# Kernel optimization log

Hardware: AMD Instinct MI355X
Metric: run time of the kernel (lower is better)

## Reference

```python
import jax, jax.numpy as jnp
import numpy as np

N = 50000      # nodes
E = 800000     # edges (before self-loops)
G = 64         # graphs
F_IN = 128     # n_attr
OUT = 128      # size_vect
NEG_SLOPE = 0.2


def setup_inputs() -> dict:
    key = jax.random.key(0)
    ks = jax.random.split(key, 48)
    def rn(i, shape, s=0.05):
        return (jax.random.normal(ks[i], shape, jnp.float32) * s)
    x = jax.random.normal(ks[0], (N, F_IN), jnp.float32)
    src = jax.random.randint(ks[1], (E,), 0, N, jnp.int32)
    dst = jax.random.randint(ks[2], (E,), 0, N, jnp.int32)
    dst = jnp.where(dst == src, (dst + 1) % N, dst)  # no pre-existing self-loops
    edge_index = jnp.stack([src, dst])
    batch = jnp.sort(jax.random.randint(ks[3], (N,), 0, G, jnp.int32))
    inp = {"x": x, "edge_index": edge_index, "batch": batch}
    # GATConv params (heads=1): W [in,out], att_src/att_dst [out], bias [out]
    dims = [(F_IN, 64), (64, 128), (128, 256)]
    for li, (di, do) in enumerate(dims, start=1):
        b = 4 + (li - 1) * 4
        inp[f"W{li}"] = rn(b, (di, do))
        inp[f"asrc{li}"] = rn(b + 1, (do,))
        inp[f"adst{li}"] = rn(b + 2, (do,))
        inp[f"b{li}"] = rn(b + 3, (do,))
    # dense tail: Linear stored as [in,out]
    dense = {"d1": (512, 256), "d2": (256, 128), "d3": (128, 64),
             "mean": (256, 64), "d4": (64, 64), "d5": (64, 128),
             "d6": (128, 256), "d7": (256, OUT)}
    i = 20
    for name, (di, do) in dense.items():
        inp[f"{name}_w"] = rn(i, (di, do))
        inp[f"{name}_b"] = rn(i + 1, (do,))
        i += 2
    return inp


def _gat_conv(x, src, dst, W, a_src, a_dst, b):
    h = x @ W                                   # [N, out]
    e = (h @ a_src)[src] + (h @ a_dst)[dst]     # [E']
    e = jnp.where(e > 0, e, NEG_SLOPE * e)      # LeakyReLU(0.2)
    m = jax.ops.segment_max(e, dst, num_segments=N)
    ex = jnp.exp(e - m[dst])
    denom = jax.ops.segment_sum(ex, dst, num_segments=N)
    alpha = ex / denom[dst]                     # segment softmax over incoming edges
    out = jax.ops.segment_sum(h[src] * alpha[:, None], dst, num_segments=N)
    return out + b


def reference(x, edge_index, batch,
              W1, asrc1, adst1, b1, W2, asrc2, adst2, b2, W3, asrc3, adst3, b3,
              d1_w, d1_b, d2_w, d2_b, d3_w, d3_b, mean_w, mean_b,
              d4_w, d4_b, d5_w, d5_b, d6_w, d6_b, d7_w, d7_b):
    ar = jnp.arange(N, dtype=edge_index.dtype)
    src = jnp.concatenate([edge_index[0], ar])  # add self-loops (PyG default)
    dst = jnp.concatenate([edge_index[1], ar])
    h = _gat_conv(x, src, dst, W1, asrc1, adst1, b1)
    h = _gat_conv(h, src, dst, W2, asrc2, adst2, b2)
    h = _gat_conv(h, src, dst, W3, asrc3, adst3, b3)   # [N, 256]
    x1 = jax.ops.segment_max(h, batch, num_segments=G)
    x2 = jax.ops.segment_sum(h, batch, num_segments=G)
    cnt = jax.ops.segment_sum(jnp.ones((N,), h.dtype), batch, num_segments=G)
    x3 = x2 / jnp.maximum(cnt, 1.0)[:, None]
    z = jnp.concatenate([x1, x2], axis=-1)              # [G, 512]
    z = jax.nn.relu(z @ d1_w + d1_b)
    z = jax.nn.relu(z @ d2_w + d2_b)
    z = jax.nn.relu(z @ d3_w + d3_b)
    z = z * jax.nn.sigmoid(x3 @ mean_w + mean_b)
    z = jax.nn.relu(z @ d4_w + d4_b)                    # dropout = identity (eval)
    z = jax.nn.relu(z @ d5_w + d5_b)
    z = jax.nn.relu(z @ d6_w + d6_b)
    return z @ d7_w + d7_b
```

## Files before the change

kernel.cpp:

```cpp
#include <hip/hip_runtime.h>
#include <hip/hip_bf16.h>
#include <math.h>

#define NN 50000
#define NE 800000
#define NEP 850000
#define NG 64
#define CAP 64

#define NBKT 49
#define BMAX 20480
#define EPB  3125
#define KE   13

typedef unsigned short u16;
typedef __attribute__((ext_vector_type(8))) short short8;
typedef __attribute__((ext_vector_type(4))) float f32x4;

__device__ __forceinline__ float bfu2f(u16 u) {
    return __uint_as_float((unsigned)u << 16);
}
__device__ __forceinline__ u16 f2bfu(float f) {
    __hip_bfloat16 h = __float2bfloat16(f);
    union { __hip_bfloat16 h; u16 u; } c; c.h = h; return c.u;
}

__device__ __forceinline__ unsigned fkey(float f) {
    unsigned u = __float_as_uint(f);
    return (u & 0x80000000u) ? ~u : (u | 0x80000000u);
}
__device__ __forceinline__ float fkey_inv(unsigned k) {
    return (k & 0x80000000u) ? __uint_as_float(k ^ 0x80000000u) : __uint_as_float(~k);
}

__global__ void k_init(int* __restrict__ deg, u16* __restrict__ srcsort,
                       int* __restrict__ poolbuf, int IB,
                       const float* __restrict__ W0, const float* __restrict__ as0, const float* __restrict__ ad0,
                       u16* __restrict__ Wb0, float* __restrict__ wa0, float* __restrict__ wb0,
                       const float* __restrict__ W1, const float* __restrict__ as1, const float* __restrict__ ad1,
                       u16* __restrict__ Wb1, float* __restrict__ wa1, float* __restrict__ wb1,
                       const float* __restrict__ W2, const float* __restrict__ as2, const float* __restrict__ ad2,
                       const float* __restrict__ b2f, const float* __restrict__ b3f,
                       u16* __restrict__ Wcb, float* __restrict__ bcv,
                       float* __restrict__ wa2c, float* __restrict__ wb2c,
                       float* __restrict__ cst) {
    __shared__ float pas[4], pbs[4];
    int tid = threadIdx.x;
    if (blockIdx.x < IB) {
        int i = blockIdx.x * 256 + tid;
        if (i < NN) {
            deg[i] = 1;
            srcsort[i << 6] = (u16)i;
        } else if (i - NN < NG * 512 + NG + 64) {
            poolbuf[i - NN] = 0;
        }
        return;
    }
    int b = blockIdx.x - IB;
    if (b < 192) {
        const float *W, *asv, *adv; u16* Wb; float *wa, *wb; int k, dout;
        if (b < 128) { W = W0; asv = as0; adv = ad0; Wb = Wb0; wa = wa0; wb = wb0; k = b;       dout = 64;  }
        else         { W = W1; asv = as1; adv = ad1; Wb = Wb1; wa = wa1; wb = wb1; k = b - 128; dout = 128; }
        float pa = 0.f, pb = 0.f;
        for (int n = tid; n < dout; n += 256) {
            float w = W[(size_t)k * dout + n];
            Wb[(size_t)k * dout + n] = f2bfu(w);
            pa += w * asv[n];
            pb += w * adv[n];
        }
#pragma unroll
        for (int off = 32; off; off >>= 1) {
            pa += __shfl_xor(pa, off);
            pb += __shfl_xor(pb, off);
        }
        if ((tid & 63) == 0) { pas[tid >> 6] = pa; pbs[tid >> 6] = pb; }
        __syncthreads();
        if (tid == 0) {
            wa[k] = pas[0] + pas[1] + pas[2] + pas[3];
            wb[k] = pbs[0] + pbs[1] + pbs[2] + pbs[3];
        }
        return;
    }
    if (b < 256) {
        int k = b - 192;
        int o = tid;
        float wc = 0.f;
        const float* wrow = W1 + (size_t)k * 128;
#pragma unroll 4
        for (int j = 0; j < 128; j++) wc += wrow[j] * W2[(size_t)j * 256 + o];
        Wcb[(size_t)k * 256 + o] = f2bfu(wc);
        float pa = wc * as2[o];
        float pb = wc * ad2[o];
#pragma unroll
        for (int off = 32; off; off >>= 1) {
            pa += __shfl_xor(pa, off);
            pb += __shfl_xor(pb, off);
        }
        if ((tid & 63) == 0) { pas[tid >> 6] = pa; pbs[tid >> 6] = pb; }
        __syncthreads();
        if (tid == 0) {
            wa2c[k] = pas[0] + pas[1] + pas[2] + pas[3];
            wb2c[k] = pbs[0] + pbs[1] + pbs[2] + pbs[3];
        }
        return;
    }
    {
        int o = tid;
        float t = 0.f;
#pragma unroll 4
        for (int j = 0; j < 128; j++) t += b2f[j] * W2[(size_t)j * 256 + o];
        bcv[o] = t + b3f[o];
        float ps = t * as2[o];
        float pt = t * ad2[o];
#pragma unroll
        for (int off = 32; off; off >>= 1) {
            ps += __shfl_xor(ps, off);
            pt += __shfl_xor(pt, off);
        }
        if ((tid & 63) == 0) { pas[tid >> 6] = ps; pbs[tid >> 6] = pt; }
        __syncthreads();
        if (tid == 0) {
            cst[0] = pas[0] + pas[1] + pas[2] + pas[3];
            cst[1] = pbs[0] + pbs[1] + pbs[2] + pbs[3];
        }
    }
}

__global__ __launch_bounds__(256) void k_bin(const int* __restrict__ src, const int* __restrict__ dst,
                                             unsigned* __restrict__ ebuf, int* __restrict__ bcur) {
    __shared__ int hist[NBKT], gbase[NBKT];
    int tid = threadIdx.x;
    int e0 = blockIdx.x * EPB;
    if (tid < NBKT) hist[tid] = 0;
    __syncthreads();
    unsigned pk[KE];
    unsigned br[KE];
#pragma unroll
    for (int k = 0; k < KE; k++) {
        int e = tid + k * 256;
        pk[k] = 0; br[k] = 0xffffffffu;
        if (e < EPB) {
            int sv = src[e0 + e];
            int dv = dst[e0 + e];
            int bkt = dv >> 10;
            int r = atomicAdd(&hist[bkt], 1);
            pk[k] = (unsigned)sv | ((unsigned)(dv & 1023) << 16);
            br[k] = ((unsigned)bkt << 16) | (unsigned)r;
        }
    }
    __syncthreads();
    if (tid < NBKT) gbase[tid] = atomicAdd(&bcur[tid], hist[tid]);
    __syncthreads();
#pragma unroll
    for (int k = 0; k < KE; k++) {
        if (br[k] != 0xffffffffu) {
            int bkt = (int)(br[k] >> 16);
            int r   = (int)(br[k] & 0xffffu);
            ebuf[(size_t)bkt * BMAX + gbase[bkt] + r] = pk[k];
        }
    }
}

template<int DIN, int DOUT, bool XF32, bool STIN, bool POOL>
__device__ __forceinline__ void gemm_body(int bx, const void* __restrict__ Xin,
                                          const u16* __restrict__ Wb,
                                          u16* __restrict__ Hb,
                                          const float* __restrict__ bias,
                                          const float* __restrict__ wav,
                                          const float* __restrict__ wbv,
                                          float* __restrict__ sout,
                                          float* __restrict__ tout,
                                          const int* __restrict__ batch,
                                          unsigned* __restrict__ x1k,
                                          float* __restrict__ x2,
                                          float* __restrict__ cnt) {
    constexpr int KS = DIN / 32;
    constexpr int CT = DOUT / 16;
    constexpr int TPW = CT / 4;
    constexpr int STRIDE = DIN + 16;
    __shared__ u16 Xs[64 * STRIDE];
    __shared__ int gID[64];
    int tid = threadIdx.x, wave = tid >> 6, lane = tid & 63;
    int quad = lane >> 4, l15 = lane & 15;
    int n0 = bx * 64;

    short8 bfr[TPW][KS];
#pragma unroll
    for (int ct = 0; ct < TPW; ct++) {
        int nb = (wave * TPW + ct) * 16 + l15;
#pragma unroll
        for (int ks = 0; ks < KS; ks++) {
            int kb = ks * 32 + quad * 8;
            short8 b;
#pragma unroll
            for (int j = 0; j < 8; j++) b[j] = (short)Wb[(size_t)(kb + j) * DOUT + nb];
            bfr[ct][ks] = b;
        }
    }

    if constexpr (POOL) {
        if (tid < 64) {
            int rg = n0 + tid;
            gID[tid] = batch[(rg < NN) ? rg : (NN - 1)];
        }
    }

    for (int c = tid; c < 64 * DIN / 8; c += 256) {
        int row = (c * 8) / DIN, col = (c * 8) % DIN;
        int rg = n0 + row; if (rg >= NN) rg = NN - 1;
        u16 v[8];
        if constexpr (XF32) {
            const float* p = (const float*)Xin + (size_t)rg * DIN + col;
            float4 f0 = *(const float4*)p;
            float4 f1 = *(const float4*)(p + 4);
            v[0] = f2bfu(f0.x); v[1] = f2bfu(f0.y); v[2] = f2bfu(f0.z); v[3] = f2bfu(f0.w);
            v[4] = f2bfu(f1.x); v[5] = f2bfu(f1.y); v[6] = f2bfu(f1.z); v[7] = f2bfu(f1.w);
            if constexpr (STIN) {
                float pa = f0.x * wav[col]     + f0.y * wav[col + 1]
                         + f0.z * wav[col + 2] + f0.w * wav[col + 3]
                         + f1.x * wav[col + 4] + f1.y * wav[col + 5]
                         + f1.z * wav[col + 6] + f1.w * wav[col + 7];
                float pb = f0.x * wbv[col]     + f0.y * wbv[col + 1]
                         + f0.z * wbv[col + 2] + f0.w * wbv[col + 3]
                         + f1.x * wbv[col + 4] + f1.y * wbv[col + 5]
                         + f1.z * wbv[col + 6] + f1.w * wbv[col + 7];
                constexpr int RT = DIN / 8;
#pragma unroll
                for (int off = RT / 2; off; off >>= 1) {
                    pa += __shfl_xor(pa, off);
                    pb += __shfl_xor(pb, off);
                }
                if ((tid & (RT - 1)) == 0 && (n0 + row) < NN) {
                    sout[n0 + row] = pa;
                    tout[n0 + row] = pb;
                }
            }
        } else {
            const u16* p = (const u16*)Xin + (size_t)rg * DIN + col;
            ushort4 a = *(const ushort4*)p;
            ushort4 b = *(const ushort4*)(p + 4);
            v[0] = a.x; v[1] = a.y; v[2] = a.z; v[3] = a.w;
            v[4] = b.x; v[5] = b.y; v[6] = b.z; v[7] = b.w;
        }
        u16* d = &Xs[row * STRIDE + col];
#pragma unroll
        for (int j = 0; j < 8; j++) d[j] = v[j];
    }
    __syncthreads();

    f32x4 acc[4][TPW];
#pragma unroll
    for (int rt = 0; rt < 4; rt++) {
        short8 afr[KS];
#pragma unroll
        for (int ks = 0; ks < KS; ks++)
            afr[ks] = *(const short8*)&Xs[(rt * 16 + l15) * STRIDE + ks * 32 + quad * 8];
#pragma unroll
        for (int ct = 0; ct < TPW; ct++) {
            f32x4 cf = {0.f, 0.f, 0.f, 0.f};
#pragma unroll
            for (int ks = 0; ks < KS; ks++)
                cf = __builtin_amdgcn_mfma_f32_16x16x32_bf16(afr[ks], bfr[ct][ks], cf, 0, 0, 0);
            if constexpr (POOL) {
                acc[rt][ct] = cf;
            } else {
                int col = (wave * TPW + ct) * 16 + l15;
                float bv = bias ? bias[col] : 0.f;
                int rbase = n0 + rt * 16 + quad * 4;
#pragma unroll
                for (int reg = 0; reg < 4; reg++) {
                    int r = rbase + reg;
                    if (r < NN) Hb[(size_t)r * DOUT + col] = f2bfu(cf[reg] + bv);
                }
            }
        }
    }

    if constexpr (POOL) {
        float bv[TPW];
#pragma unroll
        for (int ct = 0; ct < TPW; ct++) bv[ct] = bias[(wave * TPW + ct) * 16 + l15];
        int gmin = gID[0];
        int lastv = (n0 + 63 < NN) ? 63 : (NN - 1 - n0);
        int gmax = gID[lastv];
        for (int g = gmin; g <= gmax; g++) {
            float m[TPW], ss[TPW];
#pragma unroll
            for (int ct = 0; ct < TPW; ct++) { m[ct] = -INFINITY; ss[ct] = 0.f; }
#pragma unroll
            for (int rt = 0; rt < 4; rt++) {
#pragma unroll
                for (int reg = 0; reg < 4; reg++) {
                    int lr = rt * 16 + quad * 4 + reg;
                    bool ok = (n0 + lr < NN) && (gID[lr] == g);
#pragma unroll
                    for (int ct = 0; ct < TPW; ct++) {
                        float v = acc[rt][ct][reg] + bv[ct];
                        if (ok) { m[ct] = fmaxf(m[ct], v); ss[ct] += v; }
                    }
                }
            }
#pragma unroll
            for (int ct = 0; ct < TPW; ct++) {
                m[ct]  = fmaxf(m[ct],  __shfl_xor(m[ct], 16));
                ss[ct] += __shfl_xor(ss[ct], 16);
                m[ct]  = fmaxf(m[ct],  __shfl_xor(m[ct], 32));
                ss[ct] += __shfl_xor(ss[ct], 32);
            }
            if (lane < 16) {
#pragma unroll
                for (int ct = 0; ct < TPW; ct++) {
                    int col = (wave * TPW + ct) * 16 + l15;
                    if (m[ct] > -INFINITY) {
                        atomicMax(&x1k[(size_t)g * 256 + col], fkey(m[ct]));
                        atomicAdd(&x2[(size_t)g * 256 + col], ss[ct]);
                    }
                }
            }
        }
        if (tid == 0) {
            int cg = gID[0], cc = 0;
            for (int i = 0; i < 64; i++) {
                if (n0 + i >= NN) break;
                if (gID[i] != cg) { atomicAdd(&cnt[cg], (float)cc); cg = gID[i]; cc = 0; }
                cc++;
            }
            if (cc > 0) atomicAdd(&cnt[cg], (float)cc);
        }
    }
}

__global__ __launch_bounds__(256) void k_front(const unsigned* __restrict__ ebuf,
                                               const int* __restrict__ bcur,
                                               int* __restrict__ deg, u16* __restrict__ srcsort,
                                               const float* __restrict__ x_in,
                                               const u16* __restrict__ Wb0, u16* __restrict__ Hb,
                                               const float* __restrict__ wa, const float* __restrict__ wb,
                                               float* __restrict__ s, float* __restrict__ t) {
    int tid = threadIdx.x;
    if (blockIdx.x < NBKT) {
        __shared__ int cnt[1024];
        int bkt = blockIdx.x;
        int base = bkt << 10;
        for (int i = tid; i < 1024; i += 256) cnt[i] = 1;
        __syncthreads();
        int n = bcur[bkt];
        const unsigned* eb = ebuf + (size_t)bkt * BMAX;
        for (int e = tid; e < n; e += 256) {
            unsigned p = eb[e];
            int sv = (int)(p & 0xffffu);
            int dl = (int)(p >> 16);
            int pos = atomicAdd(&cnt[dl], 1);
            if (pos < CAP) srcsort[((base + dl) << 6) + pos] = (u16)sv;
        }
        __syncthreads();
        for (int i = tid; i < 1024; i += 256) {
            int node = base + i;
            if (node < NN) deg[node] = cnt[i];
        }
        return;
    }
    gemm_body<128, 64, true, true, false>(blockIdx.x - NBKT, x_in, Wb0, Hb, nullptr, wa, wb, s, t,
                                          nullptr, nullptr, nullptr, nullptr);
}

template<int DIN, int DOUT>
__global__ __launch_bounds__(256) void k_gemm_pool(const u16* __restrict__ Xin,
                                                   const u16* __restrict__ Wb,
                                                   const float* __restrict__ bias,
                                                   const int* __restrict__ batch,
                                                   unsigned* __restrict__ x1k,
                                                   float* __restrict__ x2,
                                                   float* __restrict__ cnt) {
    gemm_body<DIN, DOUT, false, false, true>(blockIdx.x, Xin, Wb, nullptr, bias,
                                             nullptr, nullptr, nullptr, nullptr,
                                             batch, x1k, x2, cnt);
}

template<bool BIAS>
__global__ void k_agg1(const int* __restrict__ deg, const u16* __restrict__ srcsort,
                       const float* __restrict__ s, const float* __restrict__ t,
                       const u16* __restrict__ Hb, const float* __restrict__ bias,
                       u16* __restrict__ OUT, const float* __restrict__ wan,
                       const float* __restrict__ wbn, const float* __restrict__ cst,
                       float* __restrict__ sout, float* __restrict__ tout) {
    constexpr int GS = 8;
    constexpr int P  = 8;
    int node = blockIdx.x * 4 + (threadIdx.x >> 6);
    int lane = threadIdx.x & 63;
    if (node >= NN) return;
    int cnt = min(deg[node], CAP);
    float tn = t[node];
    int sv = 0; float ex = 0.f;
    if (lane < cnt) {
        sv = srcsort[(node << 6) + lane];
        float e = s[sv] + tn;
        e = (e > 0.f) ? e : 0.2f * e;
        ex = expf(e);
    }
    float dsum = ex;
#pragma unroll
    for (int off = 32; off; off >>= 1) dsum += __shfl_xor(dsum, off);
    ex *= 1.f / dsum;

    int sg = lane / GS;
    int pg = lane % GS;
    float acc[8];
#pragma unroll
    for (int e = 0; e < 8; e++) acc[e] = 0.f;

    for (int q = 0; q < cnt; q += P) {
        int myq = q + sg;
        int mq = (myq < cnt) ? myq : q;
        float a = __shfl(ex, mq);
        int  idx = __shfl(sv, mq);
        if (myq >= cnt) a = 0.f;
        uint4 u = *(const uint4*)(Hb + (size_t)idx * 64 + pg * 8);
        acc[0] += a * bfu2f((u16)(u.x & 0xffff));
        acc[1] += a * bfu2f((u16)(u.x >> 16));
        acc[2] += a * bfu2f((u16)(u.y & 0xffff));
        acc[3] += a * bfu2f((u16)(u.y >> 16));
        acc[4] += a * bfu2f((u16)(u.z & 0xffff));
        acc[5] += a * bfu2f((u16)(u.z >> 16));
        acc[6] += a * bfu2f((u16)(u.w & 0xffff));
        acc[7] += a * bfu2f((u16)(u.w >> 16));
    }

#pragma unroll
    for (int step = GS; step < 64; step <<= 1) {
#pragma unroll
        for (int e = 0; e < 8; e++) acc[e] += __shfl_xor(acc[e], step);
    }
    if constexpr (BIAS) {
#pragma unroll
        for (int e = 0; e < 8; e++) acc[e] += bias[pg * 8 + e];
    }

    {
        float pa = 0.f, pb = 0.f;
#pragma unroll
        for (int e = 0; e < 8; e++) {
            pa += acc[e] * wan[pg * 8 + e];
            pb += acc[e] * wbn[pg * 8 + e];
        }
#pragma unroll
        for (int off = 32; off; off >>= 1) {
            pa += __shfl_xor(pa, off);
            pb += __shfl_xor(pb, off);
        }
        if (lane == 0) {
            float cs = 0.f, ct_ = 0.f;
            if constexpr (!BIAS) { cs = cst[0]; ct_ = cst[1]; }
            sout[node] = pa * (1.f / P) + cs;
            tout[node] = pb * (1.f / P) + ct_;
        }
    }

    if (sg == 0) {
        uint4 o;
        o.x = (unsigned)f2bfu(acc[0]) | ((unsigned)f2bfu(acc[1]) << 16);
        o.y = (unsigned)f2bfu(acc[2]) | ((unsigned)f2bfu(acc[3]) << 16);
        o.z = (unsigned)f2bfu(acc[4]) | ((unsigned)f2bfu(acc[5]) << 16);
        o.w = (unsigned)f2bfu(acc[6]) | ((unsigned)f2bfu(acc[7]) << 16);
        *(uint4*)(OUT + (size_t)node * 64 + pg * 8) = o;
    }
}

template<int DIN>
__global__ void k_aggX(const int* __restrict__ deg, const u16* __restrict__ srcsort,
                       const float* __restrict__ s, const float* __restrict__ t,
                       const u16* __restrict__ X, u16* __restrict__ OUT) {
    constexpr int GS = DIN / 8;
    constexpr int P  = 64 / GS;
    int node = blockIdx.x * 4 + (threadIdx.x >> 6);
    int lane = threadIdx.x & 63;
    if (node >= NN) return;
    int cnt = min(deg[node], CAP);
    float tn = t[node];
    int sv = 0; float ex = 0.f;
    if (lane < cnt) {
        sv = srcsort[(node << 6) + lane];
        float e = s[sv] + tn;
        e = (e > 0.f) ? e : 0.2f * e;
        ex = expf(e);
    }
    float dsum = ex;
#pragma unroll
    for (int off = 32; off; off >>= 1) dsum += __shfl_xor(dsum, off);
    ex *= 1.f / dsum;

    int sg = lane / GS;
    int pg = lane % GS;
    float acc[8];
#pragma unroll
    for (int e = 0; e < 8; e++) acc[e] = 0.f;

    for (int q = 0; q < cnt; q += P) {
        int myq = q + sg;
        int mq = (myq < cnt) ? myq : q;
        float a = __shfl(ex, mq);
        int  idx = __shfl(sv, mq);
        if (myq >= cnt) a = 0.f;
        uint4 u = *(const uint4*)(X + (size_t)idx * DIN + pg * 8);
        acc[0] += a * bfu2f((u16)(u.x & 0xffff));
        acc[1] += a * bfu2f((u16)(u.x >> 16));
        acc[2] += a * bfu2f((u16)(u.y & 0xffff));
        acc[3] += a * bfu2f((u16)(u.y >> 16));
        acc[4] += a * bfu2f((u16)(u.z & 0xffff));
        acc[5] += a * bfu2f((u16)(u.z >> 16));
        acc[6] += a * bfu2f((u16)(u.w & 0xffff));
        acc[7] += a * bfu2f((u16)(u.w >> 16));
    }

#pragma unroll
    for (int step = GS; step < 64; step <<= 1) {
#pragma unroll
        for (int e = 0; e < 8; e++) acc[e] += __shfl_xor(acc[e], step);
    }

    if (sg == 0) {
        uint4 o;
        o.x = (unsigned)f2bfu(acc[0]) | ((unsigned)f2bfu(acc[1]) << 16);
        o.y = (unsigned)f2bfu(acc[2]) | ((unsigned)f2bfu(acc[3]) << 16);
        o.z = (unsigned)f2bfu(acc[4]) | ((unsigned)f2bfu(acc[5]) << 16);
        o.w = (unsigned)f2bfu(acc[6]) | ((unsigned)f2bfu(acc[7]) << 16);
        *(uint4*)(OUT + (size_t)node * DIN + pg * 8) = o;
    }
}

template<int DIN, int DOUT, int ACT>
__device__ __forceinline__ void dense_layer(const float* __restrict__ in,
                                            const float* __restrict__ W,
                                            const float* __restrict__ B,
                                            float* __restrict__ out, int o,
                                            float* __restrict__ red) {
    constexpr int T = 1024 / DOUT;
    constexpr int KS = DIN / T;
    int oo = o % DOUT;
    int kk = o / DOUT;
    int kbase = kk * KS;
    float p0 = 0.f, p1 = 0.f, p2 = 0.f, p3 = 0.f;
#pragma unroll 4
    for (int k = 0; k < KS; k += 4) {
        p0 += in[kbase + k]     * W[(size_t)(kbase + k) * DOUT + oo];
        p1 += in[kbase + k + 1] * W[(size_t)(kbase + k + 1) * DOUT + oo];
        p2 += in[kbase + k + 2] * W[(size_t)(kbase + k + 2) * DOUT + oo];
        p3 += in[kbase + k + 3] * W[(size_t)(kbase + k + 3) * DOUT + oo];
    }
    float p = (p0 + p1) + (p2 + p3);
    red[o] = p;
    __syncthreads();
    if (o < DOUT) {
#pragma unroll
        for (int tt = 1; tt < T; tt++) p += red[oo + tt * DOUT];
        p += B[oo];
        if constexpr (ACT == 1) p = fmaxf(p, 0.f);
        else if constexpr (ACT == 2) p = 1.f / (1.f + expf(-p));
        out[oo] = p;
    }
    __syncthreads();
}

__global__ __launch_bounds__(1024) void k_tail(const unsigned* __restrict__ x1k, const float* __restrict__ x2,
                       const float* __restrict__ cnt,
                       const float* __restrict__ d1w, const float* __restrict__ d1b,
                       const float* __restrict__ d2w, const float* __restrict__ d2b,
                       const float* __restrict__ d3w, const float* __restrict__ d3b,
                       const float* __restrict__ mw,  const float* __restrict__ mb,
                       const float* __restrict__ d4w, const float* __restrict__ d4b,
                       const float* __restrict__ d5w, const float* __restrict__ d5b,
                       const float* __restrict__ d6w, const float* __restrict__ d6b,
                       const float* __restrict__ d7w, const float* __restrict__ d7b,
                       float* __restrict__ out) {
    __shared__ float z[512];
    __shared__ float A[256];
    __shared__ float Bf[256];
    __shared__ float red[1024];
    __shared__ float x3s[256];
    __shared__ float gbuf[64];
    int g = blockIdx.x, o = threadIdx.x;
    if (o < 256) {
        float c = fmaxf(cnt[g], 1.f);
        float sv = x2[(size_t)g * 256 + o];
        z[o] = fkey_inv(x1k[(size_t)g * 256 + o]);
        z[256 + o] = sv;
        x3s[o] = sv / c;
    }
    __syncthreads();
    dense_layer<512, 256, 1>(z,   d1w, d1b, A,    o, red);
    dense_layer<256, 128, 1>(A,   d2w, d2b, Bf,   o, red);
    dense_layer<128,  64, 1>(Bf,  d3w, d3b, A,    o, red);
    dense_layer<256,  64, 2>(x3s, mw,  mb,  gbuf, o, red);
    if (o < 64) A[o] *= gbuf[o];
    __syncthreads();
    dense_layer< 64,  64, 1>(A,   d4w, d4b, Bf,   o, red);
    dense_layer< 64, 128, 1>(Bf,  d5w, d5b, A,    o, red);
    dense_layer<128, 256, 1>(A,   d6w, d6b, z,    o, red);
    dense_layer<256, 128, 0>(z,   d7w, d7b, A,    o, red);
    if (o < 128) out[(size_t)g * 128 + o] = A[o];
}

extern "C" void kernel_launch(void* const* d_in, const int* in_sizes, int n_in,
                              void* d_out, int out_size, void* d_ws, size_t ws_size,
                              hipStream_t stream) {
    const float* x_in  = (const float*)d_in[0];
    const int*   ei    = (const int*)d_in[1];
    const int*   batch = (const int*)d_in[2];
    const int* src = ei;
    const int* dst = ei + NE;

    const float* Wl[3]  = { (const float*)d_in[3], (const float*)d_in[7],  (const float*)d_in[11] };
    const float* asl[3] = { (const float*)d_in[4], (const float*)d_in[8],  (const float*)d_in[12] };
    const float* adl[3] = { (const float*)d_in[5], (const float*)d_in[9],  (const float*)d_in[13] };
    const float* bl[3]  = { (const float*)d_in[6], (const float*)d_in[10], (const float*)d_in[14] };

    const float* d1w = (const float*)d_in[15]; const float* d1b = (const float*)d_in[16];
    const float* d2w = (const float*)d_in[17]; const float* d2b = (const float*)d_in[18];
    const float* d3w = (const float*)d_in[19]; const float* d3b = (const float*)d_in[20];
    const float* mw  = (const float*)d_in[21]; const float* mb  = (const float*)d_in[22];
    const float* d4w = (const float*)d_in[23]; const float* d4b = (const float*)d_in[24];
    const float* d5w = (const float*)d_in[25]; const float* d5b = (const float*)d_in[26];
    const float* d6w = (const float*)d_in[27]; const float* d6b = (const float*)d_in[28];
    const float* d7w = (const float*)d_in[29]; const float* d7b = (const float*)d_in[30];

    float* ws = (float*)d_ws;
    size_t off = 0;
    u16* Hb1 = (u16*)(ws + off); off += (size_t)NN * 32;
    u16* Xb1 = (u16*)(ws + off); off += (size_t)NN * 32;
    u16* A2  = (u16*)(ws + off); off += (size_t)NN * 32;
    u16* B3  = (u16*)(ws + off); off += (size_t)NN * 64;
    float* bcv = ws + off; off += 256;
    float* cst = ws + off; off += 64;
    unsigned* ebuf = (unsigned*)(ws + off); off += (size_t)NBKT * BMAX;
    float* sA = ws + off; off += NN;
    float* tA = ws + off; off += NN;
    float* sB = ws + off; off += NN;
    float* tB = ws + off; off += NN;
    u16* Wb0 = (u16*)(ws + off); off += (128 * 64) / 2;
    u16* Wb1 = (u16*)(ws + off); off += (64 * 128) / 2;
    u16* Wcb = (u16*)(ws + off); off += (64 * 256) / 2;
    float* wa0 = ws + off; off += 128;  float* wb0 = ws + off; off += 128;
    float* wa1 = ws + off; off += 64;   float* wb1 = ws + off; off += 64;
    float* wa2c = ws + off; off += 64;  float* wb2c = ws + off; off += 64;
    unsigned* x1k = (unsigned*)(ws + off); off += NG * 256;
    float* x2    = ws + off; off += NG * 256;
    float* cnt   = ws + off; off += NG;
    int* bcur    = (int*)(ws + off); off += 64;
    int* ip      = (int*)(ws + off);
    int* deg     = ip;               ip += NN;
    u16* srcsort = (u16*)ip;         ip += (NN * CAP) / 2;

    const int GB = (NN + 63) / 64;
    const int AB = (NN + 3) / 4;
    const int IB = (NN + NG * 512 + NG + 64 + 255) / 256;

    k_init<<<IB + 257, 256, 0, stream>>>(deg, srcsort, (int*)x1k, IB,
                                         Wl[0], asl[0], adl[0], Wb0, wa0, wb0,
                                         Wl[1], asl[1], adl[1], Wb1, wa1, wb1,
                                         Wl[2], asl[2], adl[2], bl[1], bl[2],
                                         Wcb, bcv, wa2c, wb2c, cst);
    k_bin<<<256, 256, 0, stream>>>(src, dst, ebuf, bcur);
    k_front<<<NBKT + GB, 256, 0, stream>>>(ebuf, bcur, deg, srcsort,
                                           x_in, Wb0, Hb1, wa0, wb0, sA, tA);

    k_agg1<true><<<AB, 256, 0, stream>>>(deg, srcsort, sA, tA, Hb1, bl[0],
                                         Xb1, wa1, wb1, nullptr, sB, tB);

    k_agg1<false><<<AB, 256, 0, stream>>>(deg, srcsort, sB, tB, Xb1, nullptr,
                                          A2, wa2c, wb2c, cst, sA, tA);

    k_aggX<64><<<AB, 256, 0, stream>>>(deg, srcsort, sA, tA, A2, B3);
    k_gemm_pool<64, 256><<<GB, 256, 0, stream>>>(B3, Wcb, bcv, batch, x1k, x2, cnt);

    k_tail<<<NG, 1024, 0, stream>>>(x1k, x2, cnt,
                                    d1w, d1b, d2w, d2b, d3w, d3b, mw, mb,
                                    d4w, d4b, d5w, d5b, d6w, d6b, d7w, d7b,
                                    (float*)d_out);
}
```

Baseline: 302.3 us.

## Fuse layer-3 aggregation into GEMM+pool kernel and fold binning into init

The layer-3 neighbour aggregation is merged into the GEMM+pooling kernel. Each block first gathers and softmax-weights 64 nodes' neighbours into shared memory, then runs the MFMA GEMM and graph pooling on them, so the 50000x64 bf16 intermediate is never written to or read back from global memory. The edge-binning kernel is also folded into the init kernel as extra blocks, and pooling and counter buffers are now cleared with a memset. This removes one kernel launch and a global round trip. The cost is much less parallelism in the gather phase: each wave now walks 16 nodes in sequence across only about 782 blocks, which may leave gather latency exposed.

Result: slower. 344.3 us (+13.9%).

```diff
diff --git a/kernel.cpp b/kernel.cpp
--- a/kernel.cpp
+++ b/kernel.cpp
@@ -4,7 +4,6 @@
 
 #define NN 50000
 #define NE 800000
-#define NEP 850000
 #define NG 64
 #define CAP 64
 
@@ -33,8 +32,7 @@
     return (k & 0x80000000u) ? __uint_as_float(k ^ 0x80000000u) : __uint_as_float(~k);
 }
 
-__global__ void k_init(int* __restrict__ deg, u16* __restrict__ srcsort,
-                       int* __restrict__ poolbuf, int IB,
+__global__ void k_init(int* __restrict__ deg, u16* __restrict__ srcsort, int IB,
                        const float* __restrict__ W0, const float* __restrict__ as0, const float* __restrict__ ad0,
                        u16* __restrict__ Wb0, float* __restrict__ wa0, float* __restrict__ wb0,
                        const float* __restrict__ W1, const float* __restrict__ as1, const float* __restrict__ ad1,
@@ -43,16 +41,17 @@
                        const float* __restrict__ b2f, const float* __restrict__ b3f,
                        u16* __restrict__ Wcb, float* __restrict__ bcv,
                        float* __restrict__ wa2c, float* __restrict__ wb2c,
-                       float* __restrict__ cst) {
+                       float* __restrict__ cst,
+                       const int* __restrict__ src, const int* __restrict__ dst,
+                       unsigned* __restrict__ ebuf, int* __restrict__ bcur) {
     __shared__ float pas[4], pbs[4];
+    __shared__ int hist[NBKT], gbase[NBKT];
     int tid = threadIdx.x;
     if (blockIdx.x < IB) {
         int i = blockIdx.x * 256 + tid;
         if (i < NN) {
             deg[i] = 1;
             srcsort[i << 6] = (u16)i;
-        } else if (i - NN < NG * 512 + NG + 64) {
-            poolbuf[i - NN] = 0;
         }
         return;
     }
@@ -104,7 +103,7 @@
         }
         return;
     }
-    {
+    if (b == 256) {
         int o = tid;
         float t = 0.f;
 #pragma unroll 4
@@ -123,45 +122,42 @@
             cst[0] = pas[0] + pas[1] + pas[2] + pas[3];
             cst[1] = pbs[0] + pbs[1] + pbs[2] + pbs[3];
         }
-    }
-}
-
-__global__ __launch_bounds__(256) void k_bin(const int* __restrict__ src, const int* __restrict__ dst,
-                                             unsigned* __restrict__ ebuf, int* __restrict__ bcur) {
-    __shared__ int hist[NBKT], gbase[NBKT];
-    int tid = threadIdx.x;
-    int e0 = blockIdx.x * EPB;
-    if (tid < NBKT) hist[tid] = 0;
-    __syncthreads();
-    unsigned pk[KE];
-    unsigned br[KE];
-#pragma unroll
-    for (int k = 0; k < KE; k++) {
-        int e = tid + k * 256;
-        pk[k] = 0; br[k] = 0xffffffffu;
-        if (e < EPB) {
-            int sv = src[e0 + e];
-            int dv = dst[e0 + e];
-            int bkt = dv >> 10;
-            int r = atomicAdd(&hist[bkt], 1);
-            pk[k] = (unsigned)sv | ((unsigned)(dv & 1023) << 16);
-            br[k] = ((unsigned)bkt << 16) | (unsigned)r;
-        }
-    }
-    __syncthreads();
-    if (tid < NBKT) gbase[tid] = atomicAdd(&bcur[tid], hist[tid]);
-    __syncthreads();
-#pragma unroll
-    for (int k = 0; k < KE; k++) {
-        if (br[k] != 0xffffffffu) {
-            int bkt = (int)(br[k] >> 16);
-            int r   = (int)(br[k] & 0xffffu);
-            ebuf[(size_t)bkt * BMAX + gbase[bkt] + r] = pk[k];
-        }
-    }
-}
-
-template<int DIN, int DOUT, bool XF32, bool STIN, bool POOL>
+        return;
+    }
+    {
+        int e0 = (b - 257) * EPB;
+        if (tid < NBKT) hist[tid] = 0;
+        __syncthreads();
+        unsigned pk[KE];
+        unsigned br[KE];
+#pragma unroll
+        for (int k = 0; k < KE; k++) {
+            int e = tid + k * 256;
+            pk[k] = 0; br[k] = 0xffffffffu;
+            if (e < EPB) {
+                int sv = src[e0 + e];
+                int dv = dst[e0 + e];
+                int bkt = dv >> 10;
+                int r = atomicAdd(&hist[bkt], 1);
+                pk[k] = (unsigned)sv | ((unsigned)(dv & 1023) << 16);
+                br[k] = ((unsigned)bkt << 16) | (unsigned)r;
+            }
+        }
+        __syncthreads();
+        if (tid < NBKT) gbase[tid] = atomicAdd(&bcur[tid], hist[tid]);
+        __syncthreads();
+#pragma unroll
+        for (int k = 0; k < KE; k++) {
+            if (br[k] != 0xffffffffu) {
+                int bkt = (int)(br[k] >> 16);
+                int r   = (int)(br[k] & 0xffffu);
+                ebuf[(size_t)bkt * BMAX + gbase[bkt] + r] = pk[k];
+            }
+        }
+    }
+}
+
+template<int DIN, int DOUT, bool XF32, bool STIN>
 __device__ __forceinline__ void gemm_body(int bx, const void* __restrict__ Xin,
                                           const u16* __restrict__ Wb,
                                           u16* __restrict__ Hb,
@@ -169,17 +165,12 @@
                                           const float* __restrict__ wav,
                                           const float* __restrict__ wbv,
                                           float* __restrict__ sout,
-                                          float* __restrict__ tout,
-                                          const int* __restrict__ batch,
-                                          unsigned* __restrict__ x1k,
-                                          float* __restrict__ x2,
-                                          float* __restrict__ cnt) {
+                                          float* __restrict__ tout) {
     constexpr int KS = DIN / 32;
     constexpr int CT = DOUT / 16;
     constexpr int TPW = CT / 4;
     constexpr int STRIDE = DIN + 16;
     __shared__ u16 Xs[64 * STRIDE];
-    __shared__ int gID[64];
     int tid = threadIdx.x, wave = tid >> 6, lane = tid & 63;
     int quad = lane >> 4, l15 = lane & 15;
     int n0 = bx * 64;
@@ -195,13 +186,6 @@
 #pragma unroll
             for (int j = 0; j < 8; j++) b[j] = (short)Wb[(size_t)(kb + j) * DOUT + nb];
             bfr[ct][ks] = b;
-        }
-    }
-
-    if constexpr (POOL) {
-        if (tid < 64) {
-            int rg = n0 + tid;
-            gID[tid] = batch[(rg < NN) ? rg : (NN - 1)];
         }
     }
 
@@ -248,7 +232,6 @@
     }
     __syncthreads();
 
-    f32x4 acc[4][TPW];
 #pragma unroll
     for (int rt = 0; rt < 4; rt++) {
         short8 afr[KS];
@@ -261,71 +244,14 @@
 #pragma unroll
             for (int ks = 0; ks < KS; ks++)
                 cf = __builtin_amdgcn_mfma_f32_16x16x32_bf16(afr[ks], bfr[ct][ks], cf, 0, 0, 0);
-            if constexpr (POOL) {
-                acc[rt][ct] = cf;
-            } else {
-                int col = (wave * TPW + ct) * 16 + l15;
-                float bv = bias ? bias[col] : 0.f;
-                int rbase = n0 + rt * 16 + quad * 4;
-#pragma unroll
-                for (int reg = 0; reg < 4; reg++) {
-                    int r = rbase + reg;
-                    if (r < NN) Hb[(size_t)r * DOUT + col] = f2bfu(cf[reg] + bv);
-                }
-            }
-        }
-    }
-
-    if constexpr (POOL) {
-        float bv[TPW];
-#pragma unroll
-        for (int ct = 0; ct < TPW; ct++) bv[ct] = bias[(wave * TPW + ct) * 16 + l15];
-        int gmin = gID[0];
-        int lastv = (n0 + 63 < NN) ? 63 : (NN - 1 - n0);
-        int gmax = gID[lastv];
-        for (int g = gmin; g <= gmax; g++) {
-            float m[TPW], ss[TPW];
-#pragma unroll
-            for (int ct = 0; ct < TPW; ct++) { m[ct] = -INFINITY; ss[ct] = 0.f; }
-#pragma unroll
-            for (int rt = 0; rt < 4; rt++) {
-#pragma unroll
-                for (int reg = 0; reg < 4; reg++) {
-                    int lr = rt * 16 + quad * 4 + reg;
-                    bool ok = (n0 + lr < NN) && (gID[lr] == g);
-#pragma unroll
-                    for (int ct = 0; ct < TPW; ct++) {
-                        float v = acc[rt][ct][reg] + bv[ct];
-                        if (ok) { m[ct] = fmaxf(m[ct], v); ss[ct] += v; }
-                    }
-                }
-            }
-#pragma unroll
-            for (int ct = 0; ct < TPW; ct++) {
-                m[ct]  = fmaxf(m[ct],  __shfl_xor(m[ct], 16));
-                ss[ct] += __shfl_xor(ss[ct], 16);
-                m[ct]  = fmaxf(m[ct],  __shfl_xor(m[ct], 32));
-                ss[ct] += __shfl_xor(ss[ct], 32);
-            }
-            if (lane < 16) {
-#pragma unroll
-                for (int ct = 0; ct < TPW; ct++) {
-                    int col = (wave * TPW + ct) * 16 + l15;
-                    if (m[ct] > -INFINITY) {
-                        atomicMax(&x1k[(size_t)g * 256 + col], fkey(m[ct]));
-                        atomicAdd(&x2[(size_t)g * 256 + col], ss[ct]);
-                    }
-                }
-            }
-        }
-        if (tid == 0) {
-            int cg = gID[0], cc = 0;
-            for (int i = 0; i < 64; i++) {
-                if (n0 + i >= NN) break;
-                if (gID[i] != cg) { atomicAdd(&cnt[cg], (float)cc); cg = gID[i]; cc = 0; }
-                cc++;
-            }
-            if (cc > 0) atomicAdd(&cnt[cg], (float)cc);
+            int col = (wave * TPW + ct) * 16 + l15;
+            float bv = bias ? bias[col] : 0.f;
+            int rbase = n0 + rt * 16 + quad * 4;
+#pragma unroll
+            for (int reg = 0; reg < 4; reg++) {
+                int r = rbase + reg;
+                if (r < NN) Hb[(size_t)r * DOUT + col] = f2bfu(cf[reg] + bv);
+            }
         }
     }
 }
@@ -360,21 +286,7 @@
         }
         return;
     }
-    gemm_body<128, 64, true, true, false>(blockIdx.x - NBKT, x_in, Wb0, Hb, nullptr, wa, wb, s, t,
-                                          nullptr, nullptr, nullptr, nullptr);
-}
-
-template<int DIN, int DOUT>
-__global__ __launch_bounds__(256) void k_gemm_pool(const u16* __restrict__ Xin,
-                                                   const u16* __restrict__ Wb,
-                                                   const float* __restrict__ bias,
-                                                   const int* __restrict__ batch,
-                                                   unsigned* __restrict__ x1k,
-                                                   float* __restrict__ x2,
-                                                   float* __restrict__ cnt) {
-    gemm_body<DIN, DOUT, false, false, true>(blockIdx.x, Xin, Wb, nullptr, bias,
-                                             nullptr, nullptr, nullptr, nullptr,
-                                             batch, x1k, x2, cnt);
+    gemm_body<128, 64, true, true>(blockIdx.x - NBKT, x_in, Wb0, Hb, nullptr, wa, wb, s, t);
 }
 
 template<bool BIAS>
@@ -466,65 +378,171 @@
     }
 }
 
-template<int DIN>
-__global__ void k_aggX(const int* __restrict__ deg, const u16* __restrict__ srcsort,
-                       const float* __restrict__ s, const float* __restrict__ t,
-                       const u16* __restrict__ X, u16* __restrict__ OUT) {
-    constexpr int GS = DIN / 8;
-    constexpr int P  = 64 / GS;
-    int node = blockIdx.x * 4 + (threadIdx.x >> 6);
-    int lane = threadIdx.x & 63;
-    if (node >= NN) return;
-    int cnt = min(deg[node], CAP);
-    float tn = t[node];
-    int sv = 0; float ex = 0.f;
-    if (lane < cnt) {
-        sv = srcsort[(node << 6) + lane];
-        float e = s[sv] + tn;
-        e = (e > 0.f) ? e : 0.2f * e;
-        ex = expf(e);
-    }
-    float dsum = ex;
-#pragma unroll
-    for (int off = 32; off; off >>= 1) dsum += __shfl_xor(dsum, off);
-    ex *= 1.f / dsum;
-
-    int sg = lane / GS;
-    int pg = lane % GS;
-    float acc[8];
-#pragma unroll
-    for (int e = 0; e < 8; e++) acc[e] = 0.f;
-
-    for (int q = 0; q < cnt; q += P) {
-        int myq = q + sg;
-        int mq = (myq < cnt) ? myq : q;
-        float a = __shfl(ex, mq);
-        int  idx = __shfl(sv, mq);
-        if (myq >= cnt) a = 0.f;
-        uint4 u = *(const uint4*)(X + (size_t)idx * DIN + pg * 8);
-        acc[0] += a * bfu2f((u16)(u.x & 0xffff));
-        acc[1] += a * bfu2f((u16)(u.x >> 16));
-        acc[2] += a * bfu2f((u16)(u.y & 0xffff));
-        acc[3] += a * bfu2f((u16)(u.y >> 16));
-        acc[4] += a * bfu2f((u16)(u.z & 0xffff));
-        acc[5] += a * bfu2f((u16)(u.z >> 16));
-        acc[6] += a * bfu2f((u16)(u.w & 0xffff));
-        acc[7] += a * bfu2f((u16)(u.w >> 16));
-    }
-
-#pragma unroll
-    for (int step = GS; step < 64; step <<= 1) {
-#pragma unroll
-        for (int e = 0; e < 8; e++) acc[e] += __shfl_xor(acc[e], step);
-    }
-
-    if (sg == 0) {
-        uint4 o;
-        o.x = (unsigned)f2bfu(acc[0]) | ((unsigned)f2bfu(acc[1]) << 16);
-        o.y = (unsigned)f2bfu(acc[2]) | ((unsigned)f2bfu(acc[3]) << 16);
-        o.z = (unsigned)f2bfu(acc[4]) | ((unsigned)f2bfu(acc[5]) << 16);
-        o.w = (unsigned)f2bfu(acc[6]) | ((unsigned)f2bfu(acc[7]) << 16);
-        *(uint4*)(OUT + (size_t)node * DIN + pg * 8) = o;
+__global__ __launch_bounds__(256) void k_aggemm_pool(const int* __restrict__ deg,
+                                                     const u16* __restrict__ srcsort,
+                                                     const float* __restrict__ s,
+                                                     const float* __restrict__ t,
+                                                     const u16* __restrict__ A2,
+                                                     const u16* __restrict__ Wb,
+                                                     const float* __restrict__ bias,
+                                                     const int* __restrict__ batch,
+                                                     unsigned* __restrict__ x1k,
+                                                     float* __restrict__ x2,
+                                                     float* __restrict__ cntg) {
+    constexpr int DIN = 64, DOUT = 256;
+    constexpr int KS = DIN / 32;
+    constexpr int TPW = DOUT / 16 / 4;
+    constexpr int STRIDE = DIN + 16;
+    __shared__ u16 Xs[64 * STRIDE];
+    __shared__ int gID[64];
+    int tid = threadIdx.x, wave = tid >> 6, lane = tid & 63;
+    int quad = lane >> 4, l15 = lane & 15;
+    int n0 = blockIdx.x * 64;
+
+    short8 bfr[TPW][KS];
+#pragma unroll
+    for (int ct = 0; ct < TPW; ct++) {
+        int nb = (wave * TPW + ct) * 16 + l15;
+#pragma unroll
+        for (int ks = 0; ks < KS; ks++) {
+            int kb = ks * 32 + quad * 8;
+            short8 b;
+#pragma unroll
+            for (int j = 0; j < 8; j++) b[j] = (short)Wb[(size_t)(kb + j) * DOUT + nb];
+            bfr[ct][ks] = b;
+        }
+    }
+
+    if (tid < 64) {
+        int rg = n0 + tid;
+        gID[tid] = batch[(rg < NN) ? rg : (NN - 1)];
+    }
+
+    for (int i = 0; i < 16; i++) {
+        int row = wave * 16 + i;
+        int node = n0 + row;
+        if (node < NN) {
+            int cnt = min(deg[node], CAP);
+            float tn = t[node];
+            int sv = 0; float ex = 0.f;
+            if (lane < cnt) {
+                sv = srcsort[(node << 6) + lane];
+                float e = s[sv] + tn;
+                e = (e > 0.f) ? e : 0.2f * e;
+                ex = expf(e);
+            }
+            float dsum = ex;
+#pragma unroll
+            for (int off = 32; off; off >>= 1) dsum += __shfl_xor(dsum, off);
+            ex *= 1.f / dsum;
+
+            int sg = lane / 8;
+            int pg = lane % 8;
+            float acc[8];
+#pragma unroll
+            for (int e = 0; e < 8; e++) acc[e] = 0.f;
+            for (int q = 0; q < cnt; q += 8) {
+                int myq = q + sg;
+                int mq = (myq < cnt) ? myq : q;
+                float a = __shfl(ex, mq);
+                int  idx = __shfl(sv, mq);
+                if (myq >= cnt) a = 0.f;
+                uint4 u = *(const uint4*)(A2 + (size_t)idx * 64 + pg * 8);
+                acc[0] += a * bfu2f((u16)(u.x & 0xffff));
+                acc[1] += a * bfu2f((u16)(u.x >> 16));
+                acc[2] += a * bfu2f((u16)(u.y & 0xffff));
+                acc[3] += a * bfu2f((u16)(u.y >> 16));
+                acc[4] += a * bfu2f((u16)(u.z & 0xffff));
+                acc[5] += a * bfu2f((u16)(u.z >> 16));
+                acc[6] += a * bfu2f((u16)(u.w & 0xffff));
+                acc[7] += a * bfu2f((u16)(u.w >> 16));
+            }
+#pragma unroll
+            for (int step = 8; step < 64; step <<= 1) {
+#pragma unroll
+                for (int e = 0; e < 8; e++) acc[e] += __shfl_xor(acc[e], step);
+            }
+            if (sg == 0) {
+                u16* d = &Xs[row * STRIDE + pg * 8];
+#pragma unroll
+                for (int e = 0; e < 8; e++) d[e] = f2bfu(acc[e]);
+            }
+        } else {
+            if (lane < 8) {
+                u16* d = &Xs[row * STRIDE + lane * 8];
+#pragma unroll
+                for (int e = 0; e < 8; e++) d[e] = 0;
+            }
+        }
+    }
+    __syncthreads();
+
+    f32x4 acc2[4][TPW];
+#pragma unroll
+    for (int rt = 0; rt < 4; rt++) {
+        short8 afr[KS];
+#pragma unroll
+        for (int ks = 0; ks < KS; ks++)
+            afr[ks] = *(const short8*)&Xs[(rt * 16 + l15) * STRIDE + ks * 32 + quad * 8];
+#pragma unroll
+        for (int ct = 0; ct < TPW; ct++) {
+            f32x4 cf = {0.f, 0.f, 0.f, 0.f};
+#pragma unroll
+            for (int ks = 0; ks < KS; ks++)
+                cf = __builtin_amdgcn_mfma_f32_16x16x32_bf16(afr[ks], bfr[ct][ks], cf, 0, 0, 0);
+            acc2[rt][ct] = cf;
+        }
+    }
+
+    float bv[TPW];
+#pragma unroll
+    for (int ct = 0; ct < TPW; ct++) bv[ct] = bias[(wave * TPW + ct) * 16 + l15];
+    int gmin = gID[0];
+    int lastv = (n0 + 63 < NN) ? 63 : (NN - 1 - n0);
+    int gmax = gID[lastv];
+    for (int g = gmin; g <= gmax; g++) {
+        float m[TPW], ss[TPW];
+#pragma unroll
+        for (int ct = 0; ct < TPW; ct++) { m[ct] = -INFINITY; ss[ct] = 0.f; }
+#pragma unroll
+        for (int rt = 0; rt < 4; rt++) {
+#pragma unroll
+            for (int reg = 0; reg < 4; reg++) {
+                int lr = rt * 16 + quad * 4 + reg;
+                bool ok = (n0 + lr < NN) && (gID[lr] == g);
+#pragma unroll
+                for (int ct = 0; ct < TPW; ct++) {
+                    float v = acc2[rt][ct][reg] + bv[ct];
+                    if (ok) { m[ct] = fmaxf(m[ct], v); ss[ct] += v; }
+                }
+            }
+        }
+#pragma unroll
+        for (int ct = 0; ct < TPW; ct++) {
+            m[ct]  = fmaxf(m[ct],  __shfl_xor(m[ct], 16));
+            ss[ct] += __shfl_xor(ss[ct], 16);
+            m[ct]  = fmaxf(m[ct],  __shfl_xor(m[ct], 32));
+            ss[ct] += __shfl_xor(ss[ct], 32);
+        }
+        if (lane < 16) {
+#pragma unroll
+            for (int ct = 0; ct < TPW; ct++) {
+                int col = (wave * TPW + ct) * 16 + l15;
+                if (m[ct] > -INFINITY) {
+                    atomicMax(&x1k[(size_t)g * 256 + col], fkey(m[ct]));
+                    atomicAdd(&x2[(size_t)g * 256 + col], ss[ct]);
+                }
+            }
+        }
+    }
+    if (tid == 0) {
+        int cg = gID[0], cc = 0;
+        for (int i = 0; i < 64; i++) {
+            if (n0 + i >= NN) break;
+            if (gID[i] != cg) { atomicAdd(&cntg[cg], (float)cc); cg = gID[i]; cc = 0; }
+            cc++;
+        }
+        if (cc > 0) atomicAdd(&cntg[cg], (float)cc);
     }
 }
 
@@ -628,7 +646,6 @@
     u16* Hb1 = (u16*)(ws + off); off += (size_t)NN * 32;
     u16* Xb1 = (u16*)(ws + off); off += (size_t)NN * 32;
     u16* A2  = (u16*)(ws + off); off += (size_t)NN * 32;
-    u16* B3  = (u16*)(ws + off); off += (size_t)NN * 64;
     float* bcv = ws + off; off += 256;
     float* cst = ws + off; off += 64;
     unsigned* ebuf = (unsigned*)(ws + off); off += (size_t)NBKT * BMAX;
@@ -652,14 +669,15 @@
 
     const int GB = (NN + 63) / 64;
     const int AB = (NN + 3) / 4;
-    const int IB = (NN + NG * 512 + NG + 64 + 255) / 256;
-
-    k_init<<<IB + 257, 256, 0, stream>>>(deg, srcsort, (int*)x1k, IB,
+    const int IB = (NN + 255) / 256;
+
+    hipMemsetAsync(x1k, 0, (size_t)(NG * 512 + NG + 64) * 4, stream);
+    k_init<<<IB + 513, 256, 0, stream>>>(deg, srcsort, IB,
                                          Wl[0], asl[0], adl[0], Wb0, wa0, wb0,
                                          Wl[1], asl[1], adl[1], Wb1, wa1, wb1,
                                          Wl[2], asl[2], adl[2], bl[1], bl[2],
-                                         Wcb, bcv, wa2c, wb2c, cst);
-    k_bin<<<256, 256, 0, stream>>>(src, dst, ebuf, bcur);
+                                         Wcb, bcv, wa2c, wb2c, cst,
+                                         src, dst, ebuf, bcur);
     k_front<<<NBKT + GB, 256, 0, stream>>>(ebuf, bcur, deg, srcsort,
                                            x_in, Wb0, Hb1, wa0, wb0, sA, tA);
 
@@ -669,8 +687,8 @@
     k_agg1<false><<<AB, 256, 0, stream>>>(deg, srcsort, sB, tB, Xb1, nullptr,
                                           A2, wa2c, wb2c, cst, sA, tA);
 
-    k_aggX<64><<<AB, 256, 0, stream>>>(deg, srcsort, sA, tA, A2, B3);
-    k_gemm_pool<64, 256><<<GB, 256, 0, stream>>>(B3, Wcb, bcv, batch, x1k, x2, cnt);
+    k_aggemm_pool<<<GB, 256, 0, stream>>>(deg, srcsort, sA, tA, A2, Wcb, bcv,
+                                          batch, x1k, x2, cnt);
 
     k_tail<<<NG, 1024, 0, stream>>>(x1k, x2, cnt,
                                     d1w, d1b, d2w, d2b, d3w, d3b, mw, mb,
```
